# Performance work log

Measured on AMD Instinct MI355X. Metric: run time of the kernel, lower is better.

The kernel has to match this reference:

```python
import jax, jax.numpy as jnp
import numpy as np

ALPHA = 0.2   # LeakyReLU negative slope
RATIO = 0.5   # blend ratio between attention and structural similarity
KHOP = 3      # k-hop structural similarity depth
NEG_BIG = -9e15


def _build_adj(edge, n):
    # edge: [N, D] int neighbor indices; adj[i, edge[i, d]] = 1
    rows = jnp.broadcast_to(jnp.arange(n)[:, None], edge.shape)
    return jnp.zeros((n, n), jnp.float32).at[rows, edge].set(1.0)


def _structural_similarity(adj, khop):
    # Sum of adjacency powers A + A^2 + ... + A^khop (k-hop reachability counts).
    s = adj
    p = adj
    for _ in range(khop - 1):
        p = p @ adj
        s = s + p
    return s


def _per_graph(atom, edge, W, a):
    n = atom.shape[0]
    adj = _build_adj(edge, n)
    structure = jax.nn.softmax(_structural_similarity(adj, KHOP), axis=1)
    h = atom @ W                                   # [N, F]
    f = h.shape[1]
    # a_input[i,j] = concat(h_i, h_j); a_input @ a == (h @ a1)_i + (h @ a2)_j
    src = h @ a[:f, 0]                             # [N]
    dst = h @ a[f:, 0]                             # [N]
    e = jax.nn.leaky_relu(src[:, None] + dst[None, :], ALPHA)  # [N, N]
    att = jnp.where(adj > 0, e, NEG_BIG)
    att = jax.nn.softmax(att, axis=1)
    blended = RATIO * att + (1.0 - RATIO) * structure
    return jax.nn.elu(blended @ h)                 # [N, F]


def setup_inputs() -> dict:
    key = jax.random.key(0)
    k1, k2, k3, k4 = jax.random.split(key, 4)
    B, N, D, F_IN, F_OUT = 16, 1024, 8, 128, 64
    atoms = jax.random.normal(k1, (B, N, F_IN), dtype=jnp.float32)
    edges = jax.random.randint(k2, (B, N, D), 0, N, dtype=jnp.int64)
    W = jax.random.normal(k3, (F_IN, F_OUT), dtype=jnp.float32) * 0.1
    a = jax.random.normal(k4, (2 * F_OUT, 1), dtype=jnp.float32) * 0.1
    return {"atoms": atoms, "edges": edges, "W": W, "a": a}


def reference(atoms, edges, W, a):
    return jax.vmap(_per_graph, in_axes=(0, 0, None, None))(atoms, edges, W, a)
```

## Files before the change

### kernel.cpp

```cpp
#include <hip/hip_runtime.h>

#define NN 1024
#define DG 8
#define FO 64
#define FI 128
#define LALPHA 0.2f
#define BR 16
#define SBS 257
#define AHS 68

typedef __attribute__((ext_vector_type(8))) short bf16x8;
typedef __attribute__((ext_vector_type(4))) float f32x4;

static __device__ __forceinline__ unsigned short f2bf(float x) {
  union { float f; unsigned u; } v; v.f = x;
  unsigned r = v.u + 0x7FFFu + ((v.u >> 16) & 1u);
  return (unsigned short)(r >> 16);
}
static __device__ __forceinline__ float bf2f(unsigned short h) {
  union { unsigned u; float f; } v; v.u = ((unsigned)h) << 16;
  return v.f;
}

__global__ __launch_bounds__(256) void k_prep(const float* __restrict__ atoms,
                                              const float* __restrict__ W,
                                              const float* __restrict__ a,
                                              const int* __restrict__ edges,
                                              int* __restrict__ uniq,
                                              ushort* __restrict__ hT,
                                              ushort* __restrict__ hN,
                                              float* __restrict__ srcv,
                                              float* __restrict__ dstv) {
  __shared__ float sp[16], dp[16];
  const int t = threadIdx.x, b = blockIdx.x;
  const int g = b >> 6;
  const int rbase = b * 16;

  if (t < 16) {
    sp[t] = 0.f; dp[t] = 0.f;
    const int rr = rbase + t;
    int e[DG];
#pragma unroll
    for (int s = 0; s < DG; s++) e[s] = edges[rr * DG + s];
#pragma unroll
    for (int s = 0; s < DG; s++) {
      int v = e[s];
      bool dup = false;
#pragma unroll
      for (int q = 0; q < DG; q++)
        if (q < s && e[q] == v) dup = true;
      uniq[rr * DG + s] = dup ? -1 : v;
    }
  }

  const int w = t >> 6, lane = t & 63, quad = lane >> 4, l16 = lane & 15;
  const float* __restrict__ Ar = atoms + (size_t)(rbase + l16) * FI;
  const float* __restrict__ Wc = W + w * 16 + l16;
  f32x4 acc = {0.f, 0.f, 0.f, 0.f};
#pragma unroll
  for (int kc = 0; kc < 4; kc++) {
    const int k0 = kc * 32 + quad * 8;
    float4 a0 = *(const float4*)(Ar + k0);
    float4 a1 = *(const float4*)(Ar + k0 + 4);
    float av[8] = {a0.x, a0.y, a0.z, a0.w, a1.x, a1.y, a1.z, a1.w};
    float wv[8];
#pragma unroll
    for (int e = 0; e < 8; e++) wv[e] = Wc[(k0 + e) * FO];
    bf16x8 ahi, alo, bhi, blo;
#pragma unroll
    for (int e = 0; e < 8; e++) {
      ushort h = f2bf(av[e]);
      ahi[e] = (short)h;
      alo[e] = (short)f2bf(av[e] - bf2f(h));
      ushort g2 = f2bf(wv[e]);
      bhi[e] = (short)g2;
      blo[e] = (short)f2bf(wv[e] - bf2f(g2));
    }
    acc = __builtin_amdgcn_mfma_f32_16x16x32_bf16(ahi, bhi, acc, 0, 0, 0);
    acc = __builtin_amdgcn_mfma_f32_16x16x32_bf16(ahi, blo, acc, 0, 0, 0);
    acc = __builtin_amdgcn_mfma_f32_16x16x32_bf16(alo, bhi, acc, 0, 0, 0);
  }

  const int f = w * 16 + l16;
  const float as_ = a[f], ad_ = a[FO + f];
  float ps[4], pd[4];
#pragma unroll
  for (int r = 0; r < 4; r++) {
    float v = acc[r];
    int rb = rbase + quad * 4 + r;
    ushort hv = f2bf(v);
    hT[((size_t)g * FO + f) * NN + (rb & (NN - 1))] = hv;
    hN[(size_t)rb * FO + f] = hv;
    ps[r] = v * as_;
    pd[r] = v * ad_;
  }
#pragma unroll
  for (int off = 1; off < 16; off <<= 1)
#pragma unroll
    for (int r = 0; r < 4; r++) {
      ps[r] += __shfl_xor(ps[r], off);
      pd[r] += __shfl_xor(pd[r], off);
    }
  __syncthreads();
  if (l16 == 0) {
#pragma unroll
    for (int r = 0; r < 4; r++) {
      atomicAdd(&sp[quad * 4 + r], ps[r]);
      atomicAdd(&dp[quad * 4 + r], pd[r]);
    }
  }
  __syncthreads();
  if (t < 16) {
    srcv[rbase + t] = sp[t];
    dstv[rbase + t] = dp[t];
  }
}

__global__ __launch_bounds__(256, 6) void k_fused(const int* __restrict__ uniq,
                                                  const float* __restrict__ srcv,
                                                  const float* __restrict__ dstv,
                                                  const ushort* __restrict__ hT,
                                                  const ushort* __restrict__ hN,
                                                  float* __restrict__ out) {
  __shared__ unsigned Sb[BR * SBS];
  __shared__ float attH[BR * AHS];
  __shared__ int n1[BR][DG];
  __shared__ float attw[BR][DG];

  const int t = threadIdx.x, b = blockIdx.x;
  const int g = b >> 6, rbase = (b & 63) * BR;
  const int* __restrict__ Ug = uniq + (size_t)g * NN * DG;

  for (int i = t; i < BR * SBS; i += 256) Sb[i] = 0u;
  if (t < BR * DG) n1[t >> 3][t & 7] = Ug[(rbase + (t >> 3)) * DG + (t & 7)];
  __syncthreads();

#pragma unroll
  for (int q = 0; q < 4; q++) {
    int idx = t + 256 * q;
    int r = idx >> 6, e = idx & 63;
    int j = n1[r][e >> 3];
    if (j >= 0) {
      if ((e & 7) == 0)
        atomicAdd(&Sb[r * SBS + (j >> 2)], 1u << ((j & 3) * 8));
      int k = Ug[j * DG + (e & 7)];
      if (k >= 0) {
        atomicAdd(&Sb[r * SBS + (k >> 2)], 1u << ((k & 3) * 8));
        int4 m0 = *(const int4*)(Ug + k * DG);
        int4 m1 = *(const int4*)(Ug + k * DG + 4);
        int ll[8] = {m0.x, m0.y, m0.z, m0.w, m1.x, m1.y, m1.z, m1.w};
#pragma unroll
        for (int e2 = 0; e2 < 8; e2++)
          if (ll[e2] >= 0) atomicAdd(&Sb[r * SBS + (ll[e2] >> 2)], 1u << ((ll[e2] & 3) * 8));
      }
    }
  }
  if (t < BR) {
    int r = t;
    float si = srcv[g * NN + rbase + r];
    float ev[DG];
    float m = -1e30f;
#pragma unroll
    for (int s = 0; s < DG; s++) {
      int j = n1[r][s];
      if (j >= 0) {
        float x = si + dstv[g * NN + j];
        x = x > 0.f ? x : LALPHA * x;
        ev[s] = x;
        m = fmaxf(m, x);
      } else ev[s] = -1e30f;
    }
    float sm = 0.f;
#pragma unroll
    for (int s = 0; s < DG; s++) {
      float e = (n1[r][s] >= 0) ? __expf(ev[s] - m) : 0.f;
      ev[s] = e;
      sm += e;
    }
    float inv = 1.f / sm;
#pragma unroll
    for (int s = 0; s < DG; s++) attw[r][s] = ev[s] * inv;
  }
  __syncthreads();

  {
    const int r = t >> 4, f0 = (t & 15) * 4;
    float a0 = 0.f, a1 = 0.f, a2 = 0.f, a3 = 0.f;
#pragma unroll
    for (int s = 0; s < DG; s++) {
      int j = n1[r][s];
      if (j >= 0) {
        float wgt = attw[r][s];
        uint2 hv = *(const uint2*)(hN + ((size_t)(g * NN + j)) * FO + f0);
        a0 += wgt * bf2f((ushort)(hv.x & 0xffffu));
        a1 += wgt * bf2f((ushort)(hv.x >> 16));
        a2 += wgt * bf2f((ushort)(hv.y & 0xffffu));
        a3 += wgt * bf2f((ushort)(hv.y >> 16));
      }
    }
    attH[r * AHS + f0] = a0;
    attH[r * AHS + f0 + 1] = a1;
    attH[r * AHS + f0 + 2] = a2;
    attH[r * AHS + f0 + 3] = a3;
  }
  __syncthreads();

  const int w = t >> 6, lane = t & 63, quad = lane >> 4, l16 = lane & 15;
  const ushort* __restrict__ hrow = hT + ((size_t)g * FO + w * 16 + l16) * NN;
  f32x4 acc = {0.f, 0.f, 0.f, 0.f};
  float zacc = 0.f;
#pragma unroll 8
  for (int ks = 0; ks < NN; ks += 32) {
    const int wd = l16 * SBS + (ks >> 2) + quad * 2;
    unsigned s0 = Sb[wd], s1 = Sb[wd + 1];
    float e0 = __expf((float)(s0 & 255u));
    float e1 = __expf((float)((s0 >> 8) & 255u));
    float e2 = __expf((float)((s0 >> 16) & 255u));
    float e3 = __expf((float)(s0 >> 24));
    float e4 = __expf((float)(s1 & 255u));
    float e5 = __expf((float)((s1 >> 8) & 255u));
    float e6 = __expf((float)((s1 >> 16) & 255u));
    float e7 = __expf((float)(s1 >> 24));
    zacc += (e0 + e1) + (e2 + e3) + (e4 + e5) + (e6 + e7);
    bf16x8 af;
    af[0] = (short)f2bf(e0); af[1] = (short)f2bf(e1);
    af[2] = (short)f2bf(e2); af[3] = (short)f2bf(e3);
    af[4] = (short)f2bf(e4); af[5] = (short)f2bf(e5);
    af[6] = (short)f2bf(e6); af[7] = (short)f2bf(e7);
    bf16x8 bf = *(const bf16x8*)(hrow + ks + quad * 8);
    acc = __builtin_amdgcn_mfma_f32_16x16x32_bf16(af, bf, acc, 0, 0, 0);
  }
  zacc += __shfl_xor(zacc, 16);
  zacc += __shfl_xor(zacc, 32);

#pragma unroll
  for (int r = 0; r < 4; r++) {
    const int row = quad * 4 + r;
    float Z = __shfl(zacc, row);
    float att = attH[row * AHS + w * 16 + l16];
    float v = 0.5f * att + acc[r] * (0.5f / Z);
    v = v > 0.f ? v : __expf(v) - 1.f;
    out[((size_t)(g * NN + rbase + row)) * FO + w * 16 + l16] = v;
  }
}

extern "C" void kernel_launch(void* const* d_in, const int* in_sizes, int n_in,
                              void* d_out, int out_size, void* d_ws, size_t ws_size,
                              hipStream_t stream) {
  const float* atoms = (const float*)d_in[0];
  const int* edges = (const int*)d_in[1];
  const float* W = (const float*)d_in[2];
  const float* a = (const float*)d_in[3];
  float* out = (float*)d_out;

  const int nrows = in_sizes[0] / FI;
  const int ngraph = nrows / NN;

  ushort* hT = (ushort*)d_ws;
  ushort* hN = hT + (size_t)ngraph * FO * NN;
  float* srcv = (float*)(hN + (size_t)nrows * FO);
  float* dstv = srcv + nrows;
  int* uniq = (int*)(dstv + nrows);

  k_prep<<<nrows / 16, 256, 0, stream>>>(atoms, W, a, edges, uniq, hT, hN, srcv, dstv);
  k_fused<<<ngraph * (NN / BR), 256, 0, stream>>>(uniq, srcv, dstv, hT, hN, out);
}
```

Baseline: 98.01 us.

## Split K across waves, reuse exp fragments over all columns, use exp LUT

The structural-similarity GEMM is restructured so each wave handles a quarter of the K dimension for all 64 output columns, instead of a 16-column slice over all of K. Each exp/bf16 A fragment is therefore computed once and fed to four MFMAs, rather than being recomputed by every wave. Per-count exp values come from an 80-entry shared-memory lookup table (bf16 and fp32) instead of calling __expf. Partial sums are combined through a shared-memory reduction with vectorized float4 output stores. In exchange it adds LDS use, an extra barrier and more accumulator registers, and lowers the launch-bounds occupancy hint from 6 to 4. The table also assumes a path count never exceeds 79.

```diff
diff --git a/kernel.cpp b/kernel.cpp
--- a/kernel.cpp
+++ b/kernel.cpp
@@ -7,7 +7,7 @@
 #define LALPHA 0.2f
 #define BR 16
 #define SBS 257
-#define AHS 68
+#define RDS 68
 
 typedef __attribute__((ext_vector_type(8))) short bf16x8;
 typedef __attribute__((ext_vector_type(4))) float f32x4;
@@ -116,16 +116,19 @@
   }
 }
 
-__global__ __launch_bounds__(256, 6) void k_fused(const int* __restrict__ uniq,
+__global__ __launch_bounds__(256, 4) void k_fused(const int* __restrict__ uniq,
                                                   const float* __restrict__ srcv,
                                                   const float* __restrict__ dstv,
                                                   const ushort* __restrict__ hT,
                                                   const ushort* __restrict__ hN,
                                                   float* __restrict__ out) {
   __shared__ unsigned Sb[BR * SBS];
-  __shared__ float attH[BR * AHS];
+  __shared__ __align__(16) float red[4][BR][RDS];
+  __shared__ float zred[4][16];
   __shared__ int n1[BR][DG];
   __shared__ float attw[BR][DG];
+  __shared__ float lutF[80];
+  __shared__ ushort lutB[80];
 
   const int t = threadIdx.x, b = blockIdx.x;
   const int g = b >> 6, rbase = (b & 63) * BR;
@@ -133,6 +136,12 @@
 
   for (int i = t; i < BR * SBS; i += 256) Sb[i] = 0u;
   if (t < BR * DG) n1[t >> 3][t & 7] = Ug[(rbase + (t >> 3)) * DG + (t & 7)];
+  if (t >= 128 && t < 208) {
+    int c = t - 128;
+    float e = __expf((float)c);
+    lutF[c] = e;
+    lutB[c] = f2bf(e);
+  }
   __syncthreads();
 
 #pragma unroll
@@ -183,65 +192,73 @@
   }
   __syncthreads();
 
-  {
-    const int r = t >> 4, f0 = (t & 15) * 4;
-    float a0 = 0.f, a1 = 0.f, a2 = 0.f, a3 = 0.f;
-#pragma unroll
-    for (int s = 0; s < DG; s++) {
-      int j = n1[r][s];
-      if (j >= 0) {
-        float wgt = attw[r][s];
-        uint2 hv = *(const uint2*)(hN + ((size_t)(g * NN + j)) * FO + f0);
-        a0 += wgt * bf2f((ushort)(hv.x & 0xffffu));
-        a1 += wgt * bf2f((ushort)(hv.x >> 16));
-        a2 += wgt * bf2f((ushort)(hv.y & 0xffffu));
-        a3 += wgt * bf2f((ushort)(hv.y >> 16));
-      }
-    }
-    attH[r * AHS + f0] = a0;
-    attH[r * AHS + f0 + 1] = a1;
-    attH[r * AHS + f0 + 2] = a2;
-    attH[r * AHS + f0 + 3] = a3;
-  }
-  __syncthreads();
-
-  const int w = t >> 6, lane = t & 63, quad = lane >> 4, l16 = lane & 15;
-  const ushort* __restrict__ hrow = hT + ((size_t)g * FO + w * 16 + l16) * NN;
-  f32x4 acc = {0.f, 0.f, 0.f, 0.f};
+  const int rr_ = t >> 4, f0_ = (t & 15) * 4;
+  float ah0 = 0.f, ah1 = 0.f, ah2 = 0.f, ah3 = 0.f;
+#pragma unroll
+  for (int s = 0; s < DG; s++) {
+    int j = n1[rr_][s];
+    if (j >= 0) {
+      float wgt = attw[rr_][s];
+      uint2 hv = *(const uint2*)(hN + ((size_t)(g * NN + j)) * FO + f0_);
+      ah0 += wgt * bf2f((ushort)(hv.x & 0xffffu));
+      ah1 += wgt * bf2f((ushort)(hv.x >> 16));
+      ah2 += wgt * bf2f((ushort)(hv.y & 0xffffu));
+      ah3 += wgt * bf2f((ushort)(hv.y >> 16));
+    }
+  }
+
+  const int v = t >> 6, lane = t & 63, quad = lane >> 4, l16 = lane & 15;
+  const int k0 = v * 256;
+  const ushort* __restrict__ hb = hT + ((size_t)g * FO) * NN;
+  f32x4 acc[4] = {{0.f, 0.f, 0.f, 0.f}, {0.f, 0.f, 0.f, 0.f},
+                  {0.f, 0.f, 0.f, 0.f}, {0.f, 0.f, 0.f, 0.f}};
   float zacc = 0.f;
-#pragma unroll 8
-  for (int ks = 0; ks < NN; ks += 32) {
-    const int wd = l16 * SBS + (ks >> 2) + quad * 2;
+#pragma unroll
+  for (int ks = 0; ks < 256; ks += 32) {
+    const int wd = l16 * SBS + ((k0 + ks) >> 2) + quad * 2;
     unsigned s0 = Sb[wd], s1 = Sb[wd + 1];
-    float e0 = __expf((float)(s0 & 255u));
-    float e1 = __expf((float)((s0 >> 8) & 255u));
-    float e2 = __expf((float)((s0 >> 16) & 255u));
-    float e3 = __expf((float)(s0 >> 24));
-    float e4 = __expf((float)(s1 & 255u));
-    float e5 = __expf((float)((s1 >> 8) & 255u));
-    float e6 = __expf((float)((s1 >> 16) & 255u));
-    float e7 = __expf((float)(s1 >> 24));
-    zacc += (e0 + e1) + (e2 + e3) + (e4 + e5) + (e6 + e7);
+    const int c0 = s0 & 255u, c1 = (s0 >> 8) & 255u, c2 = (s0 >> 16) & 255u, c3 = s0 >> 24;
+    const int c4 = s1 & 255u, c5 = (s1 >> 8) & 255u, c6 = (s1 >> 16) & 255u, c7 = s1 >> 24;
     bf16x8 af;
-    af[0] = (short)f2bf(e0); af[1] = (short)f2bf(e1);
-    af[2] = (short)f2bf(e2); af[3] = (short)f2bf(e3);
-    af[4] = (short)f2bf(e4); af[5] = (short)f2bf(e5);
-    af[6] = (short)f2bf(e6); af[7] = (short)f2bf(e7);
-    bf16x8 bf = *(const bf16x8*)(hrow + ks + quad * 8);
-    acc = __builtin_amdgcn_mfma_f32_16x16x32_bf16(af, bf, acc, 0, 0, 0);
+    af[0] = (short)lutB[c0]; af[1] = (short)lutB[c1];
+    af[2] = (short)lutB[c2]; af[3] = (short)lutB[c3];
+    af[4] = (short)lutB[c4]; af[5] = (short)lutB[c5];
+    af[6] = (short)lutB[c6]; af[7] = (short)lutB[c7];
+    zacc += (lutF[c0] + lutF[c1]) + (lutF[c2] + lutF[c3]) +
+            (lutF[c4] + lutF[c5]) + (lutF[c6] + lutF[c7]);
+    const ushort* hp = hb + (size_t)l16 * NN + k0 + ks + quad * 8;
+#pragma unroll
+    for (int ct = 0; ct < 4; ct++) {
+      bf16x8 bf = *(const bf16x8*)(hp + (size_t)(ct * 16) * NN);
+      acc[ct] = __builtin_amdgcn_mfma_f32_16x16x32_bf16(af, bf, acc[ct], 0, 0, 0);
+    }
   }
   zacc += __shfl_xor(zacc, 16);
   zacc += __shfl_xor(zacc, 32);
-
-#pragma unroll
-  for (int r = 0; r < 4; r++) {
-    const int row = quad * 4 + r;
-    float Z = __shfl(zacc, row);
-    float att = attH[row * AHS + w * 16 + l16];
-    float v = 0.5f * att + acc[r] * (0.5f / Z);
-    v = v > 0.f ? v : __expf(v) - 1.f;
-    out[((size_t)(g * NN + rbase + row)) * FO + w * 16 + l16] = v;
-  }
+  if (lane < 16) zred[v][lane] = zacc;
+#pragma unroll
+  for (int ct = 0; ct < 4; ct++)
+#pragma unroll
+    for (int r = 0; r < 4; r++)
+      red[v][quad * 4 + r][ct * 16 + l16] = acc[ct][r];
+  __syncthreads();
+
+  const float Z = zred[0][rr_] + zred[1][rr_] + zred[2][rr_] + zred[3][rr_];
+  const float hz = 0.5f / Z;
+  f32x4 s = *(const f32x4*)&red[0][rr_][f0_];
+  f32x4 s1v = *(const f32x4*)&red[1][rr_][f0_];
+  f32x4 s2v = *(const f32x4*)&red[2][rr_][f0_];
+  f32x4 s3v = *(const f32x4*)&red[3][rr_][f0_];
+  float o0 = 0.5f * ah0 + (s[0] + s1v[0] + s2v[0] + s3v[0]) * hz;
+  float o1 = 0.5f * ah1 + (s[1] + s1v[1] + s2v[1] + s3v[1]) * hz;
+  float o2 = 0.5f * ah2 + (s[2] + s1v[2] + s2v[2] + s3v[2]) * hz;
+  float o3 = 0.5f * ah3 + (s[3] + s1v[3] + s2v[3] + s3v[3]) * hz;
+  o0 = o0 > 0.f ? o0 : __expf(o0) - 1.f;
+  o1 = o1 > 0.f ? o1 : __expf(o1) - 1.f;
+  o2 = o2 > 0.f ? o2 : __expf(o2) - 1.f;
+  o3 = o3 > 0.f ? o3 : __expf(o3) - 1.f;
+  *(float4*)(out + ((size_t)(g * NN + rbase + rr_)) * FO + f0_) =
+      make_float4(o0, o1, o2, o3);
 }
 
 extern "C" void kernel_launch(void* const* d_in, const int* in_sizes, int n_in,
```

New measurement: 96.09 us. About the same (-2.0%).
